# Kernel optimization log

Hardware: AMD Instinct MI355X
Metric: run time of the kernel (lower is better)

Reference implementation:

```python
import jax, jax.numpy as jnp
import numpy as np
import math

D_MODEL = 512
D_HEAD = 64
N_HEADS = D_MODEL // D_HEAD  # 8
COND = 768
K = 7        # neighborhood kernel size
EPS = 1e-6


def _rope_freqs():
    # RoPE(dim=d_head//2, n_heads): freqs geometric in [pi, 10*pi), shape [n_heads, d_head//4]
    dim = D_HEAD // 2
    n = N_HEADS * dim // 2
    freqs = jnp.exp(jnp.linspace(math.log(math.pi), math.log(10.0 * math.pi), n + 1)[:-1])
    return freqs.reshape(dim // 2, N_HEADS).T  # [nh, d_head//4]


def _rms_norm(x, scale, eps):
    mean_sq = jnp.mean(x * x, axis=-1, keepdims=True)
    return x * (scale * jax.lax.rsqrt(mean_sq + eps))


def _apply_rotary(x, theta):
    # rotate first 2*d dims of head dim, leave the rest untouched
    d = theta.shape[-1]
    x1, x2, rest = x[..., :d], x[..., d:2 * d], x[..., 2 * d:]
    cos, sin = jnp.cos(theta), jnp.sin(theta)
    return jnp.concatenate([x1 * cos - x2 * sin, x2 * cos + x1 * sin, rest], axis=-1)


def _nb_idx(L, k):
    # NATTEN border handling: window shifts (clamps) so every query sees exactly k keys
    i = np.arange(L)
    start = np.clip(i - k // 2, 0, L - k)
    return jnp.asarray(start[:, None] + np.arange(k)[None, :])  # [L, k]


def setup_inputs() -> dict:
    key = jax.random.key(0)
    ks = jax.random.split(key, 7)
    N, H, W = 2, 32, 32
    x = jax.random.normal(ks[0], (N, H, W, D_MODEL), jnp.float32)
    pos = jax.random.uniform(ks[1], (N, H, W, 1), jnp.float32, -1.0, 1.0)
    cond = jax.random.normal(ks[2], (N, COND), jnp.float32)
    w_cond = jax.random.normal(ks[3], (D_MODEL, COND), jnp.float32) * 0.02
    w_qkv = jax.random.normal(ks[4], (3 * D_MODEL, D_MODEL), jnp.float32) * 0.02
    scale = jnp.full((N_HEADS,), 10.0, jnp.float32)
    w_out = jax.random.normal(ks[5], (D_MODEL, D_MODEL), jnp.float32) * 0.02
    return {"x": x, "pos": pos, "cond": cond, "w_cond": w_cond,
            "w_qkv": w_qkv, "scale": scale, "w_out": w_out}


def reference(x, pos, cond, w_cond, w_qkv, scale, w_out):
    N, H, W, C = x.shape
    skip = x
    # AdaRMSNorm: rms_norm(x, linear(cond) + 1)
    norm_scale = cond @ w_cond.T + 1.0                  # [N, C]
    xn = _rms_norm(x, norm_scale[:, None, None, :], EPS)
    # qkv projection -> [3, N, nh, H, W, e]
    qkv = (xn @ w_qkv.T).reshape(N, H, W, 3, N_HEADS, D_HEAD)
    qkv = qkv.transpose(3, 0, 4, 1, 2, 5)
    q, k, v = qkv[0], qkv[1], qkv[2]                    # [N, nh, H, W, e]
    # cosine-sim scaling
    sq = jnp.sqrt(scale)[:, None, None, None]           # [nh,1,1,1]
    q = q * (sq * jax.lax.rsqrt(jnp.sum(q * q, -1, keepdims=True) + 1e-6))
    k = k * (sq * jax.lax.rsqrt(jnp.sum(k * k, -1, keepdims=True) + 1e-6))
    # RoPE
    theta = pos[..., None, :] * _rope_freqs()           # [N,H,W,nh,e/4]
    theta = jnp.moveaxis(theta, -2, -4)                 # [N,nh,H,W,e/4]
    q = _apply_rotary(q, theta)
    k = _apply_rotary(k, theta)
    # 2D neighborhood attention (NATTEN, dilation 1)
    ih, iw = _nb_idx(H, K), _nb_idx(W, K)
    Knb = k[:, :, ih][:, :, :, :, iw]                   # [N,nh,H,K,W,K,e]
    Vnb = v[:, :, ih][:, :, :, :, iw]
    qk = jnp.einsum('ncije,nciajbe->ncijab', q, Knb)    # [N,nh,H,W,K,K]
    a = jax.nn.softmax(qk.reshape(N, N_HEADS, H, W, K * K), axis=-1)
    a = a.reshape(N, N_HEADS, H, W, K, K)
    o = jnp.einsum('ncijab,nciajbe->ncije', a, Vnb)     # [N,nh,H,W,e]
    o = o.transpose(0, 2, 3, 1, 4).reshape(N, H, W, C)
    return o @ w_out.T + skip
```

## Files before the change

kernel.cpp:

```cpp
#include <hip/hip_runtime.h>

typedef unsigned short u16;
typedef unsigned int u32;
typedef __bf16 bf16x8 __attribute__((ext_vector_type(8)));
typedef float f32x4 __attribute__((ext_vector_type(4)));

__device__ __forceinline__ float bf2f(u16 v) {
    union { u32 u; float f; } c; c.u = ((u32)v) << 16; return c.f;
}
__device__ __forceinline__ u16 f2bf(float f) {
    union { float f; u32 u; } c; c.f = f;
    u32 u = c.u + 0x7fffu + ((c.u >> 16) & 1u);
    return (u16)(u >> 16);
}

__global__ __launch_bounds__(256) void setup_kernel(
    const float* __restrict__ cond, const float* __restrict__ w_cond,
    const float* __restrict__ x, float* __restrict__ ns, float* __restrict__ inv)
{
    int lane = threadIdx.x & 63;
    int b = blockIdx.x;
    if (b < 256) {
        int wid = b * 4 + (threadIdx.x >> 6);
        int n = wid >> 9, c = wid & 511;
        const float* cp = cond + n * 768;
        const float* wp = w_cond + (size_t)c * 768;
        float s = 0.f;
        #pragma unroll
        for (int j = 0; j < 12; j++)
            s += cp[lane + j * 64] * wp[lane + j * 64];
        #pragma unroll
        for (int d = 1; d < 64; d <<= 1) s += __shfl_xor(s, d);
        if (lane == 0) ns[wid] = s + 1.f;
    } else {
        int p = (b - 256) * 4 + (threadIdx.x >> 6);
        const float* xp = x + (size_t)p * 512;
        float s = 0.f;
        #pragma unroll
        for (int j = 0; j < 8; j++) { float v = xp[lane + j * 64]; s += v * v; }
        #pragma unroll
        for (int d = 1; d < 64; d <<= 1) s += __shfl_xor(s, d);
        if (lane == 0) inv[p] = rsqrtf(s * (1.f / 512.f) + 1e-6f);
    }
}

__global__ __launch_bounds__(256) void convert_kernel(
    const float* __restrict__ x, const float* __restrict__ ns, const float* __restrict__ inv,
    const float* __restrict__ w_qkv, const float* __restrict__ w_out,
    u16* __restrict__ xn, u16* __restrict__ wqkvb, u16* __restrict__ woutb)
{
    int b = blockIdx.x;
    const float* src; u16* dst; size_t i4;
    bool rms = false;
    if (b < 1024)      { src = x;     dst = xn;    i4 = (size_t)(b)        * 1024 + threadIdx.x * 4; rms = true; }
    else if (b < 1792) { src = w_qkv; dst = wqkvb; i4 = (size_t)(b - 1024) * 1024 + threadIdx.x * 4; }
    else               { src = w_out; dst = woutb; i4 = (size_t)(b - 1792) * 1024 + threadIdx.x * 4; }
    float4 v = *(const float4*)(src + i4);
    if (rms) {
        int p = (int)(i4 >> 9), c = (int)(i4 & 511);
        float iv = inv[p];
        float4 nv = *(const float4*)(ns + (p >> 10) * 512 + c);
        v.x *= nv.x * iv; v.y *= nv.y * iv; v.z *= nv.z * iv; v.w *= nv.w * iv;
    }
    ushort4 o; o.x = f2bf(v.x); o.y = f2bf(v.y); o.z = f2bf(v.z); o.w = f2bf(v.w);
    *(ushort4*)(dst + i4) = o;
}

template<bool OUT_BF16, bool ADD_SKIP>
__global__ __launch_bounds__(256) void gemm_bt(
    const u16* __restrict__ A, const u16* __restrict__ B,
    float* __restrict__ Cf, u16* __restrict__ Cb, const float* __restrict__ skip,
    int N, int K)
{
    __shared__ __align__(16) u16 As[64][40];
    __shared__ __align__(16) u16 Bs[64][40];
    int tid = threadIdx.x;
    int lane = tid & 63;
    int w = tid >> 6;
    int wm = w >> 1, wn = w & 1;
    int bm = blockIdx.x * 64, bn = blockIdx.y * 64;
    int lrow = tid >> 2, lc8 = (tid & 3) * 8;

    f32x4 zero = {0.f, 0.f, 0.f, 0.f};
    f32x4 acc[2][2];
    acc[0][0] = zero; acc[0][1] = zero; acc[1][0] = zero; acc[1][1] = zero;

    const u16* Ap = A + (size_t)(bm + lrow) * K + lc8;
    const u16* Bp = B + (size_t)(bn + lrow) * K + lc8;
    int r = lane & 15, kq = (lane >> 4) * 8;

    for (int k0 = 0; k0 < K; k0 += 32) {
        *(uint4*)&As[lrow][lc8] = *(const uint4*)(Ap + k0);
        *(uint4*)&Bs[lrow][lc8] = *(const uint4*)(Bp + k0);
        __syncthreads();
        #pragma unroll
        for (int ri = 0; ri < 2; ri++) {
            bf16x8 af = *(const bf16x8*)&As[wm * 32 + ri * 16 + r][kq];
            #pragma unroll
            for (int ci = 0; ci < 2; ci++) {
                bf16x8 bfr = *(const bf16x8*)&Bs[wn * 32 + ci * 16 + r][kq];
                acc[ri][ci] = __builtin_amdgcn_mfma_f32_16x16x32_bf16(af, bfr, acc[ri][ci], 0, 0, 0);
            }
        }
        __syncthreads();
    }

    #pragma unroll
    for (int ri = 0; ri < 2; ri++)
    #pragma unroll
    for (int ci = 0; ci < 2; ci++) {
        int col = bn + wn * 32 + ci * 16 + (lane & 15);
        int row0 = bm + wm * 32 + ri * 16 + (lane >> 4) * 4;
        #pragma unroll
        for (int reg = 0; reg < 4; reg++) {
            size_t idx = (size_t)(row0 + reg) * N + col;
            float v = acc[ri][ci][reg];
            if (ADD_SKIP) v += skip[idx];
            if (OUT_BF16) Cb[idx] = f2bf(v);
            else Cf[idx] = v;
        }
    }
}

__global__ __launch_bounds__(256) void rope_plane_kernel(
    const u16* __restrict__ qkvb, const float* __restrict__ pos, const float* __restrict__ scale,
    u16* __restrict__ qp, u16* __restrict__ kp, u16* __restrict__ vp)
{
    int lane = threadIdx.x & 63;
    int wid = blockIdx.x * 4 + (threadIdx.x >> 6);
    int qk = wid >> 14;
    int rem = wid & 16383;
    int h = rem & 7, p = rem >> 3;
    float v = bf2f(qkvb[(size_t)p * 1536 + qk * 512 + h * 64 + lane]);
    float res = v;
    if (qk < 2) {
        float ss = v * v;
        #pragma unroll
        for (int d = 1; d < 64; d <<= 1) ss += __shfl_xor(ss, d);
        float sc = sqrtf(scale[h]) * rsqrtf(ss + 1e-6f);
        v *= sc;
        float partner = __shfl_xor(v, 16);
        res = v;
        if (lane < 32) {
            int t = lane & 15;
            float fr = 3.14159265358979323846f * expf((float)(t * 8 + h) * (2.302585092994046f / 128.f));
            float th = pos[p] * fr;
            float cs = cosf(th), sn = sinf(th);
            res = (lane < 16) ? (v * cs - partner * sn) : (v * cs + partner * sn);
        }
    }
    u16* plane = (qk == 0) ? qp : (qk == 1) ? kp : vp;
    size_t dst = ((size_t)((p >> 10) * 8 + h) * 1024 + (p & 1023)) * 64 + lane;
    plane[dst] = f2bf(res);
}

__global__ __launch_bounds__(256) void attn_mfma(
    const u16* __restrict__ qp, const u16* __restrict__ kp, const u16* __restrict__ vp,
    u16* __restrict__ ob)
{
    __shared__ __align__(16) u16 Kb[208 * 72];
    __shared__ __align__(16) u16 Sb[64 * 232];

    int tid = threadIdx.x, lane = tid & 63, w = tid >> 6;
    int bx = blockIdx.x;
    int n = bx >> 7, h = (bx >> 4) & 7, t = bx & 15;
    int ti = (t >> 2) * 8, tj = (t & 3) * 8;
    int r0 = min(max(ti - 3, 0), 18), c0 = min(max(tj - 3, 0), 18);
    const u16* qpl = qp + ((size_t)(n * 8 + h) << 16);
    const u16* kpl = kp + ((size_t)(n * 8 + h) << 16);
    const u16* vpl = vp + ((size_t)(n * 8 + h) << 16);

    for (int g = tid; g < 1568; g += 256) {
        int nb = g >> 3, k8 = (g & 7) << 3;
        int ar = nb / 14, ac = nb - ar * 14;
        *(uint4*)&Kb[nb * 72 + k8] =
            *(const uint4*)&kpl[(size_t)((r0 + ar) * 32 + c0 + ac) * 64 + k8];
    }
    __syncthreads();

    int m = lane & 15, quad = lane >> 4;
    {
        int r = w * 16 + m;
        int tok = (ti + (r >> 3)) * 32 + (tj + (r & 7));
        bf16x8 qf0 = *(const bf16x8*)&qpl[(size_t)tok * 64 + quad * 8];
        bf16x8 qf1 = *(const bf16x8*)&qpl[(size_t)tok * 64 + 32 + quad * 8];
        _Float16* sp = (_Float16*)Sb;
        #pragma unroll
        for (int nt = 0; nt < 13; nt++) {
            f32x4 acc = {0.f, 0.f, 0.f, 0.f};
            bf16x8 b0 = *(const bf16x8*)&Kb[(nt * 16 + m) * 72 + quad * 8];
            bf16x8 b1 = *(const bf16x8*)&Kb[(nt * 16 + m) * 72 + 32 + quad * 8];
            acc = __builtin_amdgcn_mfma_f32_16x16x32_bf16(qf0, b0, acc, 0, 0, 0);
            acc = __builtin_amdgcn_mfma_f32_16x16x32_bf16(qf1, b1, acc, 0, 0, 0);
            #pragma unroll
            for (int reg = 0; reg < 4; reg++)
                sp[(w * 16 + quad * 4 + reg) * 232 + nt * 16 + m] = (_Float16)acc[reg];
        }
    }
    __syncthreads();

    for (int g = tid; g < 1568; g += 256) {
        int nb = g >> 3, k8 = (g & 7) << 3;
        int ar = nb / 14, ac = nb - ar * 14;
        uint4 v4 = *(const uint4*)&vpl[(size_t)((r0 + ar) * 32 + c0 + ac) * 64 + k8];
        u32 uu[4] = {v4.x, v4.y, v4.z, v4.w};
        #pragma unroll
        for (int e = 0; e < 4; e++) {
            Kb[(k8 + 2 * e) * 234 + nb]     = (u16)(uu[e] & 0xffff);
            Kb[(k8 + 2 * e + 1) * 234 + nb] = (u16)(uu[e] >> 16);
        }
    }
    for (int g = tid; g < 1792; g += 256) {
        int d = g / 28, nb = 196 + (g - d * 28);
        Kb[d * 234 + nb] = 0;
    }

    {
        int l16 = lane & 15, g4 = lane >> 4;
        #pragma unroll
        for (int it = 0; it < 4; it++) {
            int rr = w * 16 + it * 4 + g4;
            int i2 = ti + (rr >> 3), j2 = tj + (rr & 7);
            int alo = min(max(i2 - 3, 0), 25) - r0;
            int blo = min(max(j2 - 3, 0), 25) - c0;
            const _Float16* sp = (const _Float16*)&Sb[rr * 232];
            float vals[14];
            float mx = -1e30f;
            #pragma unroll
            for (int c = 0; c < 14; c++) {
                int col = l16 + c * 16;
                float v = -1e30f;
                if (col < 196) {
                    int ar = col / 14, ac = col - ar * 14;
                    if (ar >= alo && ar < alo + 7 && ac >= blo && ac < blo + 7)
                        v = (float)sp[col];
                }
                vals[c] = v; mx = fmaxf(mx, v);
            }
            #pragma unroll
            for (int d = 1; d < 16; d <<= 1) mx = fmaxf(mx, __shfl_xor(mx, d));
            float s = 0.f;
            #pragma unroll
            for (int c = 0; c < 14; c++) {
                float e = (vals[c] > -1e29f) ? expf(vals[c] - mx) : 0.f;
                vals[c] = e; s += e;
            }
            #pragma unroll
            for (int d = 1; d < 16; d <<= 1) s += __shfl_xor(s, d);
            float rs = __frcp_rn(s);
            u16* pp = &Sb[rr * 232];
            #pragma unroll
            for (int c = 0; c < 14; c++)
                pp[l16 + c * 16] = f2bf(vals[c] * rs);
        }
    }
    __syncthreads();

    f32x4 oacc[4];
    #pragma unroll
    for (int nt = 0; nt < 4; nt++) { f32x4 z = {0.f,0.f,0.f,0.f}; oacc[nt] = z; }
    #pragma unroll
    for (int ks = 0; ks < 7; ks++) {
        bf16x8 pa = *(const bf16x8*)&Sb[(w * 16 + m) * 232 + ks * 32 + quad * 8];
        #pragma unroll
        for (int nt = 0; nt < 4; nt++) {
            int ad = (nt * 16 + m) * 234 + ks * 32 + quad * 8;
            union { u32 u[4]; bf16x8 v; } vb;
            vb.u[0] = *(const u32*)&Kb[ad];
            vb.u[1] = *(const u32*)&Kb[ad + 2];
            vb.u[2] = *(const u32*)&Kb[ad + 4];
            vb.u[3] = *(const u32*)&Kb[ad + 6];
            oacc[nt] = __builtin_amdgcn_mfma_f32_16x16x32_bf16(pa, vb.v, oacc[nt], 0, 0, 0);
        }
    }
    #pragma unroll
    for (int nt = 0; nt < 4; nt++) {
        #pragma unroll
        for (int reg = 0; reg < 4; reg++) {
            int rr = w * 16 + quad * 4 + reg;
            int tok = (ti + (rr >> 3)) * 32 + (tj + (rr & 7));
            ob[(size_t)(n * 1024 + tok) * 512 + h * 64 + nt * 16 + m] = f2bf(oacc[nt][reg]);
        }
    }
}

extern "C" void kernel_launch(void* const* d_in, const int* in_sizes, int n_in,
                              void* d_out, int out_size, void* d_ws, size_t ws_size,
                              hipStream_t stream)
{
    const float *x = nullptr, *pos = nullptr, *cond = nullptr, *w_cond = nullptr,
                *w_qkv = nullptr, *scale = nullptr, *w_out = nullptr;
    for (int i = 0; i < n_in; i++) {
        switch (in_sizes[i]) {
            case 1048576: x      = (const float*)d_in[i]; break;
            case 2048:    pos    = (const float*)d_in[i]; break;
            case 1536:    cond   = (const float*)d_in[i]; break;
            case 393216:  w_cond = (const float*)d_in[i]; break;
            case 786432:  w_qkv  = (const float*)d_in[i]; break;
            case 8:       scale  = (const float*)d_in[i]; break;
            case 262144:  w_out  = (const float*)d_in[i]; break;
            default: break;
        }
    }
    float* out = (float*)d_out;

    char* ws = (char*)d_ws;
    float* ns    = (float*)ws;
    float* inv   = (float*)(ws + 4096);
    u16*   qkvb  = (u16*)(ws + 12288);
    u16*   xn    = (u16*)(ws + 12288 + 6291456);
    u16*   wqkvb = (u16*)(ws + 12288 + 8388608);
    u16*   woutb = (u16*)(ws + 12288 + 9961472);
    u16*   qp    = (u16*)(ws + 12288 + 10485760);
    u16*   kp    = (u16*)(ws + 12288 + 12582912);
    u16*   vp    = (u16*)(ws + 12288 + 14680064);
    u16*   ob    = (u16*)(ws + 12288 + 16777216);

    setup_kernel<<<768, 256, 0, stream>>>(cond, w_cond, x, ns, inv);
    convert_kernel<<<2048, 256, 0, stream>>>(x, ns, inv, w_qkv, w_out, xn, wqkvb, woutb);
    gemm_bt<true, false><<<dim3(32, 24), 256, 0, stream>>>(xn, wqkvb, nullptr, qkvb, nullptr, 1536, 512);
    rope_plane_kernel<<<12288, 256, 0, stream>>>(qkvb, pos, scale, qp, kp, vp);
    attn_mfma<<<256, 256, 0, stream>>>(qp, kp, vp, ob);
    gemm_bt<false, true><<<dim3(32, 8), 256, 0, stream>>>(ob, woutb, out, nullptr, x, 512, 512);
}
```

Baseline: 121.1 us.

## Fuse q/k normalization and RoPE into QKV GEMM epilogue, drop rope kernel

The QKV projection GEMM now performs per-head cosine normalization (row sum-of-squares reduced across the two wave columns via shared memory) and rotary embedding in its epilogue. It writes bf16 q/k/v planes directly in head-major layout. This removes the separate rope_plane kernel launch and the round trip of the intermediate qkv buffer through global memory. The cost is a heavier epilogue with an extra barrier and scattered 2-byte stores into the plane layout.

Measured after the change: 115.2 us. 1.05x faster.

```diff
diff --git a/kernel.cpp b/kernel.cpp
--- a/kernel.cpp
+++ b/kernel.cpp
@@ -66,11 +66,97 @@
     *(ushort4*)(dst + i4) = o;
 }
 
-template<bool OUT_BF16, bool ADD_SKIP>
-__global__ __launch_bounds__(256) void gemm_bt(
+__global__ __launch_bounds__(256) void gemm_qkv(
     const u16* __restrict__ A, const u16* __restrict__ B,
-    float* __restrict__ Cf, u16* __restrict__ Cb, const float* __restrict__ skip,
-    int N, int K)
+    const float* __restrict__ pos, const float* __restrict__ scale,
+    u16* __restrict__ qp, u16* __restrict__ kp, u16* __restrict__ vp)
+{
+    __shared__ __align__(16) u16 As[64][40];
+    __shared__ __align__(16) u16 Bs[64][40];
+    int tid = threadIdx.x;
+    int lane = tid & 63;
+    int w = tid >> 6;
+    int wm = w >> 1, wn = w & 1;
+    int bm = blockIdx.x * 64, bn = blockIdx.y * 64;
+    int qk = blockIdx.y >> 3, h = blockIdx.y & 7;
+    int lrow = tid >> 2, lc8 = (tid & 3) * 8;
+
+    f32x4 zero = {0.f, 0.f, 0.f, 0.f};
+    f32x4 acc[2][2];
+    acc[0][0] = zero; acc[0][1] = zero; acc[1][0] = zero; acc[1][1] = zero;
+
+    const u16* Ap = A + (size_t)(bm + lrow) * 512 + lc8;
+    const u16* Bp = B + (size_t)(bn + lrow) * 512 + lc8;
+    int m = lane & 15, quad = lane >> 4, kq = quad * 8;
+
+    for (int k0 = 0; k0 < 512; k0 += 32) {
+        *(uint4*)&As[lrow][lc8] = *(const uint4*)(Ap + k0);
+        *(uint4*)&Bs[lrow][lc8] = *(const uint4*)(Bp + k0);
+        __syncthreads();
+        #pragma unroll
+        for (int ri = 0; ri < 2; ri++) {
+            bf16x8 af = *(const bf16x8*)&As[wm * 32 + ri * 16 + m][kq];
+            #pragma unroll
+            for (int ci = 0; ci < 2; ci++) {
+                bf16x8 bfr = *(const bf16x8*)&Bs[wn * 32 + ci * 16 + m][kq];
+                acc[ri][ci] = __builtin_amdgcn_mfma_f32_16x16x32_bf16(af, bfr, acc[ri][ci], 0, 0, 0);
+            }
+        }
+        __syncthreads();
+    }
+
+    float invn[2][4];
+    if (qk < 2) {
+        float* red = (float*)As;
+        #pragma unroll
+        for (int ri = 0; ri < 2; ri++)
+        #pragma unroll
+        for (int reg = 0; reg < 4; reg++) {
+            float pa = acc[ri][0][reg] * acc[ri][0][reg]
+                     + acc[ri][1][reg] * acc[ri][1][reg];
+            #pragma unroll
+            for (int d = 1; d < 16; d <<= 1) pa += __shfl_xor(pa, d);
+            if (m == 0) red[(wm * 32 + ri * 16 + quad * 4 + reg) * 2 + wn] = pa;
+        }
+        __syncthreads();
+        float sq = sqrtf(scale[h]);
+        #pragma unroll
+        for (int ri = 0; ri < 2; ri++)
+        #pragma unroll
+        for (int reg = 0; reg < 4; reg++) {
+            int rl = wm * 32 + ri * 16 + quad * 4 + reg;
+            invn[ri][reg] = sq * rsqrtf(red[rl * 2] + red[rl * 2 + 1] + 1e-6f);
+        }
+    }
+    u16* plane = (qk == 0) ? qp : (qk == 1) ? kp : vp;
+    float fr = 3.14159265358979323846f * expf((float)(m * 8 + h) * (2.302585092994046f / 128.f));
+    #pragma unroll
+    for (int ri = 0; ri < 2; ri++)
+    #pragma unroll
+    for (int reg = 0; reg < 4; reg++) {
+        int rl = wm * 32 + ri * 16 + quad * 4 + reg;
+        int p = bm + rl;
+        size_t basep = ((size_t)((p >> 10) * 8 + h) * 1024 + (p & 1023)) * 64;
+        float v0 = acc[ri][0][reg], v1 = acc[ri][1][reg];
+        if (qk < 2) {
+            float ivn = invn[ri][reg];
+            v0 *= ivn; v1 *= ivn;
+            if (wn == 0) {
+                float th = pos[p] * fr;
+                float cs = cosf(th), sn = sinf(th);
+                float o0 = v0 * cs - v1 * sn;
+                float o1 = v1 * cs + v0 * sn;
+                v0 = o0; v1 = o1;
+            }
+        }
+        plane[basep + wn * 32 + m]      = f2bf(v0);
+        plane[basep + wn * 32 + 16 + m] = f2bf(v1);
+    }
+}
+
+__global__ __launch_bounds__(256) void gemm_out(
+    const u16* __restrict__ A, const u16* __restrict__ B,
+    float* __restrict__ C, const float* __restrict__ skip, int N, int K)
 {
     __shared__ __align__(16) u16 As[64][40];
     __shared__ __align__(16) u16 Bs[64][40];
@@ -114,44 +200,9 @@
         #pragma unroll
         for (int reg = 0; reg < 4; reg++) {
             size_t idx = (size_t)(row0 + reg) * N + col;
-            float v = acc[ri][ci][reg];
-            if (ADD_SKIP) v += skip[idx];
-            if (OUT_BF16) Cb[idx] = f2bf(v);
-            else Cf[idx] = v;
-        }
-    }
-}
-
-__global__ __launch_bounds__(256) void rope_plane_kernel(
-    const u16* __restrict__ qkvb, const float* __restrict__ pos, const float* __restrict__ scale,
-    u16* __restrict__ qp, u16* __restrict__ kp, u16* __restrict__ vp)
-{
-    int lane = threadIdx.x & 63;
-    int wid = blockIdx.x * 4 + (threadIdx.x >> 6);
-    int qk = wid >> 14;
-    int rem = wid & 16383;
-    int h = rem & 7, p = rem >> 3;
-    float v = bf2f(qkvb[(size_t)p * 1536 + qk * 512 + h * 64 + lane]);
-    float res = v;
-    if (qk < 2) {
-        float ss = v * v;
-        #pragma unroll
-        for (int d = 1; d < 64; d <<= 1) ss += __shfl_xor(ss, d);
-        float sc = sqrtf(scale[h]) * rsqrtf(ss + 1e-6f);
-        v *= sc;
-        float partner = __shfl_xor(v, 16);
-        res = v;
-        if (lane < 32) {
-            int t = lane & 15;
-            float fr = 3.14159265358979323846f * expf((float)(t * 8 + h) * (2.302585092994046f / 128.f));
-            float th = pos[p] * fr;
-            float cs = cosf(th), sn = sinf(th);
-            res = (lane < 16) ? (v * cs - partner * sn) : (v * cs + partner * sn);
-        }
-    }
-    u16* plane = (qk == 0) ? qp : (qk == 1) ? kp : vp;
-    size_t dst = ((size_t)((p >> 10) * 8 + h) * 1024 + (p & 1023)) * 64 + lane;
-    plane[dst] = f2bf(res);
+            C[idx] = acc[ri][ci][reg] + skip[idx];
+        }
+    }
 }
 
 __global__ __launch_bounds__(256) void attn_mfma(
@@ -307,19 +358,17 @@
     char* ws = (char*)d_ws;
     float* ns    = (float*)ws;
     float* inv   = (float*)(ws + 4096);
-    u16*   qkvb  = (u16*)(ws + 12288);
-    u16*   xn    = (u16*)(ws + 12288 + 6291456);
-    u16*   wqkvb = (u16*)(ws + 12288 + 8388608);
-    u16*   woutb = (u16*)(ws + 12288 + 9961472);
-    u16*   qp    = (u16*)(ws + 12288 + 10485760);
-    u16*   kp    = (u16*)(ws + 12288 + 12582912);
-    u16*   vp    = (u16*)(ws + 12288 + 14680064);
-    u16*   ob    = (u16*)(ws + 12288 + 16777216);
+    u16*   xn    = (u16*)(ws + 12288);
+    u16*   wqkvb = (u16*)(ws + 12288 + 2097152);
+    u16*   woutb = (u16*)(ws + 12288 + 3670016);
+    u16*   qp    = (u16*)(ws + 12288 + 4194304);
+    u16*   kp    = (u16*)(ws + 12288 + 6291456);
+    u16*   vp    = (u16*)(ws + 12288 + 8388608);
+    u16*   ob    = (u16*)(ws + 12288 + 10485760);
 
     setup_kernel<<<768, 256, 0, stream>>>(cond, w_cond, x, ns, inv);
     convert_kernel<<<2048, 256, 0, stream>>>(x, ns, inv, w_qkv, w_out, xn, wqkvb, woutb);
-    gemm_bt<true, false><<<dim3(32, 24), 256, 0, stream>>>(xn, wqkvb, nullptr, qkvb, nullptr, 1536, 512);
-    rope_plane_kernel<<<12288, 256, 0, stream>>>(qkvb, pos, scale, qp, kp, vp);
+    gemm_qkv<<<dim3(32, 24), 256, 0, stream>>>(xn, wqkvb, pos, scale, qp, kp, vp);
     attn_mfma<<<256, 256, 0, stream>>>(qp, kp, vp, ob);
-    gemm_bt<false, true><<<dim3(32, 8), 256, 0, stream>>>(ob, woutb, out, nullptr, x, 512, 512);
-}
+    gemm_out<<<dim3(32, 8), 256, 0, stream>>>(ob, woutb, out, x, 512, 512);
+}
```
